# Optimization experiments

Hardware: AMD Instinct MI355X
Metric: run time of the kernel (lower is better)

## Reference

```python
import jax, jax.numpy as jnp
import numpy as np

B, Q, H, V = 32, 180, 768, 19004


def setup_inputs() -> dict:
    key = jax.random.key(0)
    k1, k2, k3, k4 = jax.random.split(key, 4)
    output_tokens = jax.random.normal(k1, (B, Q, H), dtype=jnp.float32)
    W_embed = jax.random.normal(k2, (V, H), dtype=jnp.float32) * 0.02
    b_embed = jax.random.normal(k3, (V,), dtype=jnp.float32) * 0.02
    parcel_ids = jax.random.randint(k4, (V,), 0, Q, dtype=jnp.int32)
    return {"output_tokens": output_tokens, "W_embed": W_embed,
            "b_embed": b_embed, "parcel_ids": parcel_ids}


def reference(output_tokens, W_embed, b_embed, parcel_ids):
    # embed: Linear(hidden_dim -> num_hemi_voxels): [B, Q, V]
    pred = jnp.einsum('bqh,vh->bqv', output_tokens, W_embed) + b_embed
    # movedim(1, -1): [B, V, Q]
    pred = jnp.moveaxis(pred, 1, -1)
    # parcel_mask: one-hot [V, Q] (each voxel assigned to exactly one parcel)
    num_q = output_tokens.shape[1]
    mask = jax.nn.one_hot(parcel_ids, num_q, dtype=pred.dtype)  # [V, Q]
    # multiply by mask and sum over parcel/query axis -> [B, V]
    return jnp.sum(pred * mask, axis=-1)
```

## Files before the change

### kernel.cpp

```cpp
#include <hip/hip_runtime.h>
#include <hip/hip_bf16.h>

#define BB 32
#define QQ 180
#define HH 768
#define VV 19004
#define VB 64
#define KH 384
#define SB 19008
#define MAXDESC 480
#define STRIDE 392
#define NB 80
#define CH 238

#define WS_H      0
#define WS_BASE   65536
#define WS_NTOT   131072
#define WS_DESC   132096
#define WS_SORTED 140288
#define WS_POSOF  217088
#define WS_RES    294912

typedef __attribute__((ext_vector_type(8))) short short8v;
typedef __attribute__((ext_vector_type(4))) float f32x4;

__device__ __forceinline__ short f2bf(float f) {
    unsigned u = __builtin_bit_cast(unsigned, f);
    u += 0x7FFFu + ((u >> 16) & 1u);
    return (short)(u >> 16);
}

__global__ void hist_k(const int* __restrict__ pid, int* __restrict__ h) {
    __shared__ int lc[QQ];
    const int t = threadIdx.x, b = blockIdx.x;
    if (t < QQ) lc[t] = 0;
    __syncthreads();
    const int v = b * CH + t;
    if (t < CH && v < VV) atomicAdd(&lc[pid[v]], 1);
    __syncthreads();
    if (t < QQ) h[b * QQ + t] = lc[t];
}

__global__ void scan_k(const int* __restrict__ h, int* __restrict__ base,
                       int4* __restrict__ desc, int* __restrict__ ntot) {
    __shared__ int s1[256];
    __shared__ int s2[256];
    const int t = threadIdx.x;
    int c = 0;
    if (t < QQ)
        for (int i = 0; i < NB; ++i) c += h[i * QQ + t];
    s1[t] = c;
    __syncthreads();
    for (int off = 1; off < 256; off <<= 1) {
        int a = (t >= off) ? s1[t - off] : 0;
        __syncthreads();
        s1[t] += a;
        __syncthreads();
    }
    const int qs = s1[t] - c;
    const int nch = (c + VB - 1) / VB;
    s2[t] = nch;
    __syncthreads();
    for (int off = 1; off < 256; off <<= 1) {
        int a = (t >= off) ? s2[t - off] : 0;
        __syncthreads();
        s2[t] += a;
        __syncthreads();
    }
    if (t < QQ) {
        const int cb = s2[t] - nch;
        for (int j = 0; j < nch; ++j)
            desc[cb + j] = make_int4(t, qs + j * VB, min(VB, c - j * VB), 0);
        int run = qs;
        for (int i = 0; i < NB; ++i) {
            base[i * QQ + t] = run;
            run += h[i * QQ + t];
        }
    }
    if (t == 255) *ntot = s2[255];
}

__global__ void scatter_k(const int* __restrict__ pid, const int* __restrict__ base,
                          int* __restrict__ sorted, int* __restrict__ posOf) {
    __shared__ int cur[QQ];
    const int t = threadIdx.x, b = blockIdx.x;
    if (t < QQ) cur[t] = base[b * QQ + t];
    __syncthreads();
    const int v = b * CH + t;
    if (t < CH && v < VV) {
        const int q = pid[v];
        const int pos = atomicAdd(&cur[q], 1);
        sorted[pos] = v;
        posOf[v] = pos;
    }
}

__launch_bounds__(256)
__global__ void main_k(const float* __restrict__ OT, const float* __restrict__ W,
                       const int* __restrict__ sorted, const int4* __restrict__ desc,
                       const int* __restrict__ ntot, float* __restrict__ res) {
    const int nt = *ntot;
    const int bid = blockIdx.x;
    const int ci = bid >> 1;
    if (ci >= nt) return;
    const int kh = bid & 1;
    const int4 d = desc[ci];
    const int q     = __builtin_amdgcn_readfirstlane(d.x);
    const int start = __builtin_amdgcn_readfirstlane(d.y);
    const int len   = __builtin_amdgcn_readfirstlane(d.z);
    const int tid = threadIdx.x;

    __shared__ short OTlds[BB * STRIDE];

    {
        const int r = tid >> 3;
        const int o = tid & 7;
        const float* src = OT + ((size_t)r * QQ + q) * HH + kh * KH + o * 8;
        short* dst = &OTlds[r * STRIDE + o * 8];
#pragma unroll
        for (int it = 0; it < 6; ++it) {
            const float4 f0 = *(const float4*)(src + it * 64);
            const float4 f1 = *(const float4*)(src + it * 64 + 4);
            short8v s;
            s[0] = f2bf(f0.x); s[1] = f2bf(f0.y); s[2] = f2bf(f0.z); s[3] = f2bf(f0.w);
            s[4] = f2bf(f1.x); s[5] = f2bf(f1.y); s[6] = f2bf(f1.z); s[7] = f2bf(f1.w);
            *(short8v*)(dst + it * 64) = s;
        }
    }

    const int lane = tid & 63;
    const int w = tid >> 6;
    const int co = lane & 15;
    const int kq = lane >> 4;
    const int vl = 16 * w + co;
    const int vg = sorted[start + min(vl, len - 1)];
    const float4* wp4 = (const float4*)(W + (size_t)vg * HH + kh * KH + kq * 8);
    const short* a0 = &OTlds[co * STRIDE + kq * 8];

    float4 wf[24];
#pragma unroll
    for (int kk = 0; kk < 12; ++kk) {
        wf[2 * kk]     = wp4[kk * 8];
        wf[2 * kk + 1] = wp4[kk * 8 + 1];
    }

    __syncthreads();

    f32x4 acc0 = {0.f, 0.f, 0.f, 0.f};
    f32x4 acc1 = {0.f, 0.f, 0.f, 0.f};
#pragma unroll
    for (int kk = 0; kk < 12; ++kk) {
        const float4 wf0 = wf[2 * kk];
        const float4 wf1 = wf[2 * kk + 1];
        short8v bf;
        bf[0] = f2bf(wf0.x); bf[1] = f2bf(wf0.y); bf[2] = f2bf(wf0.z); bf[3] = f2bf(wf0.w);
        bf[4] = f2bf(wf1.x); bf[5] = f2bf(wf1.y); bf[6] = f2bf(wf1.z); bf[7] = f2bf(wf1.w);
        const short8v a0v = *(const short8v*)(a0 + kk * 32);
        const short8v a1v = *(const short8v*)(a0 + 16 * STRIDE + kk * 32);
        acc0 = __builtin_amdgcn_mfma_f32_16x16x32_bf16(a0v, bf, acc0, 0, 0, 0);
        acc1 = __builtin_amdgcn_mfma_f32_16x16x32_bf16(a1v, bf, acc1, 0, 0, 0);
    }

    if (vl < len) {
        float* rp = res + (size_t)(kh * BB) * SB + start + vl;
#pragma unroll
        for (int r2 = 0; r2 < 4; ++r2) {
            rp[(size_t)(kq * 4 + r2) * SB]      = acc0[r2];
            rp[(size_t)(16 + kq * 4 + r2) * SB] = acc1[r2];
        }
    }
}

__global__ void combine_k(const float* __restrict__ res, const int* __restrict__ posOf,
                          const float* __restrict__ bias, float* __restrict__ out) {
    const int v = blockIdx.x * 256 + threadIdx.x;
    if (v >= VV) return;
    const int b = blockIdx.y;
    const int pos = posOf[v];
    const float s = res[(size_t)b * SB + pos] + res[(size_t)(BB + b) * SB + pos];
    out[(size_t)b * VV + v] = s + bias[v];
}

extern "C" void kernel_launch(void* const* d_in, const int* in_sizes, int n_in,
                              void* d_out, int out_size, void* d_ws, size_t ws_size,
                              hipStream_t stream) {
    const float* OT   = (const float*)d_in[0];
    const float* W    = (const float*)d_in[1];
    const float* bias = (const float*)d_in[2];
    const int*   pid  = (const int*)d_in[3];
    float* out = (float*)d_out;

    char* ws = (char*)d_ws;
    int*   h      = (int*)(ws + WS_H);
    int*   base   = (int*)(ws + WS_BASE);
    int*   ntot   = (int*)(ws + WS_NTOT);
    int4*  desc   = (int4*)(ws + WS_DESC);
    int*   sorted = (int*)(ws + WS_SORTED);
    int*   posOf  = (int*)(ws + WS_POSOF);
    float* res    = (float*)(ws + WS_RES);

    hist_k<<<NB, 256, 0, stream>>>(pid, h);
    scan_k<<<1, 256, 0, stream>>>(h, base, desc, ntot);
    scatter_k<<<NB, 256, 0, stream>>>(pid, base, sorted, posOf);

    main_k<<<2 * MAXDESC, 256, 0, stream>>>(OT, W, sorted, desc, ntot, res);

    combine_k<<<dim3((VV + 255) / 256, BB), 256, 0, stream>>>(res, posOf, bias, out);
}
```

Before: 45.07 us.

## Split reduction into four K slices and process two voxel tiles per block

The main GEMM kernel now splits the hidden dimension into four 192-wide slices instead of two 384-wide slices. Each block covers a 128-voxel parcel chunk as two 64-voxel sub-tiles, so the output-token tile staged in LDS is reused across twice as many voxels. The combine kernel now sums four partial results instead of two. In exchange, the partial-result buffer and combine-pass traffic double, and chunks with fewer than 128 voxels carry more wasted lanes.

```diff
diff --git a/kernel.cpp b/kernel.cpp
--- a/kernel.cpp
+++ b/kernel.cpp
@@ -5,11 +5,11 @@
 #define QQ 180
 #define HH 768
 #define VV 19004
-#define VB 64
-#define KH 384
+#define PB 128
+#define KQ 192
 #define SB 19008
-#define MAXDESC 480
-#define STRIDE 392
+#define MAXP 360
+#define ST 200
 #define NB 80
 #define CH 238
 
@@ -58,7 +58,7 @@
         __syncthreads();
     }
     const int qs = s1[t] - c;
-    const int nch = (c + VB - 1) / VB;
+    const int nch = (c + PB - 1) / PB;
     s2[t] = nch;
     __syncthreads();
     for (int off = 1; off < 256; off <<= 1) {
@@ -70,7 +70,7 @@
     if (t < QQ) {
         const int cb = s2[t] - nch;
         for (int j = 0; j < nch; ++j)
-            desc[cb + j] = make_int4(t, qs + j * VB, min(VB, c - j * VB), 0);
+            desc[cb + j] = make_int4(t, qs + j * PB, min(PB, c - j * PB), 0);
         int run = qs;
         for (int i = 0; i < NB; ++i) {
             base[i * QQ + t] = run;
@@ -99,26 +99,26 @@
 __global__ void main_k(const float* __restrict__ OT, const float* __restrict__ W,
                        const int* __restrict__ sorted, const int4* __restrict__ desc,
                        const int* __restrict__ ntot, float* __restrict__ res) {
-    const int nt = *ntot;
+    const int np = *ntot;
     const int bid = blockIdx.x;
-    const int ci = bid >> 1;
-    if (ci >= nt) return;
-    const int kh = bid & 1;
-    const int4 d = desc[ci];
+    const int p = bid >> 2;
+    if (p >= np) return;
+    const int kh = bid & 3;
+    const int4 d = desc[p];
     const int q     = __builtin_amdgcn_readfirstlane(d.x);
     const int start = __builtin_amdgcn_readfirstlane(d.y);
     const int len   = __builtin_amdgcn_readfirstlane(d.z);
     const int tid = threadIdx.x;
 
-    __shared__ short OTlds[BB * STRIDE];
+    __shared__ short OTlds[BB * ST];
 
     {
         const int r = tid >> 3;
         const int o = tid & 7;
-        const float* src = OT + ((size_t)r * QQ + q) * HH + kh * KH + o * 8;
-        short* dst = &OTlds[r * STRIDE + o * 8];
-#pragma unroll
-        for (int it = 0; it < 6; ++it) {
+        const float* src = OT + ((size_t)r * QQ + q) * HH + kh * KQ + o * 8;
+        short* dst = &OTlds[r * ST + o * 8];
+#pragma unroll
+        for (int it = 0; it < 3; ++it) {
             const float4 f0 = *(const float4*)(src + it * 64);
             const float4 f1 = *(const float4*)(src + it * 64 + 4);
             short8v s;
@@ -132,41 +132,61 @@
     const int w = tid >> 6;
     const int co = lane & 15;
     const int kq = lane >> 4;
-    const int vl = 16 * w + co;
-    const int vg = sorted[start + min(vl, len - 1)];
-    const float4* wp4 = (const float4*)(W + (size_t)vg * HH + kh * KH + kq * 8);
-    const short* a0 = &OTlds[co * STRIDE + kq * 8];
-
-    float4 wf[24];
-#pragma unroll
-    for (int kk = 0; kk < 12; ++kk) {
-        wf[2 * kk]     = wp4[kk * 8];
-        wf[2 * kk + 1] = wp4[kk * 8 + 1];
-    }
-
-    __syncthreads();
-
-    f32x4 acc0 = {0.f, 0.f, 0.f, 0.f};
-    f32x4 acc1 = {0.f, 0.f, 0.f, 0.f};
-#pragma unroll
-    for (int kk = 0; kk < 12; ++kk) {
-        const float4 wf0 = wf[2 * kk];
-        const float4 wf1 = wf[2 * kk + 1];
-        short8v bf;
-        bf[0] = f2bf(wf0.x); bf[1] = f2bf(wf0.y); bf[2] = f2bf(wf0.z); bf[3] = f2bf(wf0.w);
-        bf[4] = f2bf(wf1.x); bf[5] = f2bf(wf1.y); bf[6] = f2bf(wf1.z); bf[7] = f2bf(wf1.w);
-        const short8v a0v = *(const short8v*)(a0 + kk * 32);
-        const short8v a1v = *(const short8v*)(a0 + 16 * STRIDE + kk * 32);
-        acc0 = __builtin_amdgcn_mfma_f32_16x16x32_bf16(a0v, bf, acc0, 0, 0, 0);
-        acc1 = __builtin_amdgcn_mfma_f32_16x16x32_bf16(a1v, bf, acc1, 0, 0, 0);
-    }
-
-    if (vl < len) {
-        float* rp = res + (size_t)(kh * BB) * SB + start + vl;
+    const int vlA = 16 * w + co;
+    const int vlB = 64 + vlA;
+    const int vgA = sorted[start + min(vlA, len - 1)];
+    const int vgB = sorted[start + min(vlB, len - 1)];
+    const float4* wpA = (const float4*)(W + (size_t)vgA * HH + kh * KQ + kq * 8);
+    const float4* wpB = (const float4*)(W + (size_t)vgB * HH + kh * KQ + kq * 8);
+
+    float4 wfA[12], wfB[12];
+#pragma unroll
+    for (int kk = 0; kk < 6; ++kk) {
+        wfA[2 * kk]     = wpA[kk * 8];
+        wfA[2 * kk + 1] = wpA[kk * 8 + 1];
+        wfB[2 * kk]     = wpB[kk * 8];
+        wfB[2 * kk + 1] = wpB[kk * 8 + 1];
+    }
+
+    __syncthreads();
+
+    const short* a0p = &OTlds[co * ST + kq * 8];
+    f32x4 accA0 = {0.f,0.f,0.f,0.f}, accA1 = {0.f,0.f,0.f,0.f};
+    f32x4 accB0 = {0.f,0.f,0.f,0.f}, accB1 = {0.f,0.f,0.f,0.f};
+#pragma unroll
+    for (int kk = 0; kk < 6; ++kk) {
+        const short8v a0v = *(const short8v*)(a0p + kk * 32);
+        const short8v a1v = *(const short8v*)(a0p + 16 * ST + kk * 32);
+        short8v bfA, bfB;
+        {
+            const float4 f0 = wfA[2 * kk], f1 = wfA[2 * kk + 1];
+            bfA[0]=f2bf(f0.x); bfA[1]=f2bf(f0.y); bfA[2]=f2bf(f0.z); bfA[3]=f2bf(f0.w);
+            bfA[4]=f2bf(f1.x); bfA[5]=f2bf(f1.y); bfA[6]=f2bf(f1.z); bfA[7]=f2bf(f1.w);
+        }
+        {
+            const float4 f0 = wfB[2 * kk], f1 = wfB[2 * kk + 1];
+            bfB[0]=f2bf(f0.x); bfB[1]=f2bf(f0.y); bfB[2]=f2bf(f0.z); bfB[3]=f2bf(f0.w);
+            bfB[4]=f2bf(f1.x); bfB[5]=f2bf(f1.y); bfB[6]=f2bf(f1.z); bfB[7]=f2bf(f1.w);
+        }
+        accA0 = __builtin_amdgcn_mfma_f32_16x16x32_bf16(a0v, bfA, accA0, 0, 0, 0);
+        accA1 = __builtin_amdgcn_mfma_f32_16x16x32_bf16(a1v, bfA, accA1, 0, 0, 0);
+        accB0 = __builtin_amdgcn_mfma_f32_16x16x32_bf16(a0v, bfB, accB0, 0, 0, 0);
+        accB1 = __builtin_amdgcn_mfma_f32_16x16x32_bf16(a1v, bfB, accB1, 0, 0, 0);
+    }
+
+    float* rpl = res + (size_t)(kh * BB) * SB + start;
+    if (vlA < len) {
 #pragma unroll
         for (int r2 = 0; r2 < 4; ++r2) {
-            rp[(size_t)(kq * 4 + r2) * SB]      = acc0[r2];
-            rp[(size_t)(16 + kq * 4 + r2) * SB] = acc1[r2];
+            rpl[(size_t)(kq * 4 + r2) * SB + vlA]      = accA0[r2];
+            rpl[(size_t)(16 + kq * 4 + r2) * SB + vlA] = accA1[r2];
+        }
+    }
+    if (vlB < len) {
+#pragma unroll
+        for (int r2 = 0; r2 < 4; ++r2) {
+            rpl[(size_t)(kq * 4 + r2) * SB + vlB]      = accB0[r2];
+            rpl[(size_t)(16 + kq * 4 + r2) * SB + vlB] = accB1[r2];
         }
     }
 }
@@ -177,7 +197,10 @@
     if (v >= VV) return;
     const int b = blockIdx.y;
     const int pos = posOf[v];
-    const float s = res[(size_t)b * SB + pos] + res[(size_t)(BB + b) * SB + pos];
+    const float s = res[(size_t)b * SB + pos]
+                  + res[(size_t)(BB + b) * SB + pos]
+                  + res[(size_t)(2 * BB + b) * SB + pos]
+                  + res[(size_t)(3 * BB + b) * SB + pos];
     out[(size_t)b * VV + v] = s + bias[v];
 }
 
@@ -203,7 +226,7 @@
     scan_k<<<1, 256, 0, stream>>>(h, base, desc, ntot);
     scatter_k<<<NB, 256, 0, stream>>>(pid, base, sorted, posOf);
 
-    main_k<<<2 * MAXDESC, 256, 0, stream>>>(OT, W, sorted, desc, ntot, res);
+    main_k<<<4 * MAXP, 256, 0, stream>>>(OT, W, sorted, desc, ntot, res);
 
     combine_k<<<dim3((VV + 255) / 256, BB), 256, 0, stream>>>(res, posOf, bias, out);
 }
```

Result: slower. 49.93 us (+10.8%).
